# Kernel optimization log

Measured on AMD Instinct MI355X. Metric: run time of the kernel, lower is better.

## Reference

```python
import jax, jax.numpy as jnp
import numpy as np

R_GAS = 8314.46261815324   # Cantera gas constant, J/(kmol K)
ONE_ATM = 101325.0
B, S, NR = 2048, 100, 800
POLY = 5


def setup_inputs() -> dict:
    key = jax.random.key(0)
    ks = jax.random.split(key, 11)
    T = jax.random.uniform(ks[0], (B, 1), minval=300.0, maxval=2500.0)
    P = ONE_ATM * jax.random.uniform(ks[1], (B, 1), minval=0.5, maxval=2.0)
    Y = jax.random.uniform(ks[2], (B, S), minval=0.01, maxval=1.0)
    TPY = jnp.concatenate([T, P, Y], axis=1)
    molecular_weights = jax.random.uniform(ks[3], (S, 1), minval=2.0, maxval=100.0)
    # NASA-7 coefficients with realistic per-column magnitudes
    scales = jnp.array([1.0, 1e-3, 1e-6, 1e-9, 1e-12, 1e3, 1.0])
    base = jnp.array([3.5, 0.0, 0.0, 0.0, 0.0, 0.0, 5.0])
    nasa_low = jax.random.normal(ks[4], (S, 7)) * scales + base
    nasa_high = jax.random.normal(ks[5], (S, 7)) * scales + base
    efficiencies_coeffs = jax.random.uniform(ks[6], (S, NR), minval=0.0, maxval=2.0)
    is_three_body = (jax.random.uniform(ks[7], (NR,)) < 0.3).astype(jnp.float32)
    # positive poly coefficients so viscosity/conductivity/diffusion stay > 0
    species_viscosities_poly = jax.random.uniform(ks[8], (POLY, S), minval=1e-6, maxval=1e-5)
    thermal_conductivity_poly = jax.random.uniform(ks[9], (POLY, S), minval=1e-4, maxval=1e-3)
    binary_diff_coeffs_poly = jax.random.uniform(ks[10], (POLY, S * S), minval=1e-7, maxval=1e-6)
    return {
        'TPY': TPY,
        'molecular_weights': molecular_weights,
        'nasa_low': nasa_low,
        'nasa_high': nasa_high,
        'efficiencies_coeffs': efficiencies_coeffs,
        'is_three_body': is_three_body,
        'species_viscosities_poly': species_viscosities_poly,
        'thermal_conductivity_poly': thermal_conductivity_poly,
        'binary_diff_coeffs_poly': binary_diff_coeffs_poly,
    }


def _forward(TPY, mw, nasa_low, nasa_high, eff, i3b, visc_poly, cond_poly, bdiff_poly):
    n_sp = mw.shape[0]
    # ---- set_states: state variables ----
    T = jnp.clip(TPY[:, 0:1], 200.0, None)            # [B,1]
    logT = jnp.log(T)
    P = TPY[:, 1:2]
    Y = jnp.clip(TPY[:, 2:], 0.0, None)
    Y = Y / Y.sum(axis=1, keepdims=True)
    mean_W = 1.0 / (Y @ (1.0 / mw))                   # [B,1]
    rho = P / R_GAS / T * mean_W                      # mass density
    X = Y * mean_W / mw.T                             # mole fractions
    C = Y * rho / mw.T                                # molar concentrations
    mask = (T <= 1000.0).astype(T.dtype)              # [B,1] NASA branch select
    # ---- cp (NASA poly) ----
    cp_T = jnp.concatenate([T**0, T, T**2, T**3, T**4], axis=1)
    cp = (cp_T @ nasa_low[:, :5].T) * mask + (cp_T @ nasa_high[:, :5].T) * (1.0 - mask)
    cp_mole = (R_GAS * cp * X).sum(axis=1)
    # ---- enthalpy ----
    H_T = jnp.concatenate([T**0, T / 2, T**2 / 3, T**3 / 4, T**4 / 5, 1.0 / T], axis=1)
    H = ((H_T @ nasa_low[:, :6].T) * mask + (H_T @ nasa_high[:, :6].T) * (1.0 - mask)) * R_GAS * T
    h = H / mw.T
    enthalpy_mass = (h * Y).sum(axis=1)
    # ---- entropy ----
    idx = jnp.array([0, 1, 2, 3, 4, 6])
    S_T = jnp.concatenate([logT, T, T**2 / 2, T**3 / 3, T**4 / 4, T**0], axis=1)
    S0 = ((S_T @ nasa_low[:, idx].T) * mask + (S_T @ nasa_high[:, idx].T) * (1.0 - mask)) * R_GAS
    S_sp = S0 - R_GAS * jnp.log(X) - R_GAS * jnp.log(P / ONE_ATM)
    s = S_sp / mw.T
    entropy_mass = (s * Y).sum(axis=1)
    # ---- third-body effective concentrations ----
    C_M = C @ eff                                     # [B,NR]
    C_M2 = C_M * i3b + (1.0 - i3b)
    # ---- update_transport: viscosity (Wilke mixing) ----
    poly_order = visc_poly.shape[0]
    trans_T = jnp.concatenate([logT**i for i in range(poly_order - 1, -1, -1)], axis=1)
    sp_visc = trans_T @ visc_poly                     # [B,S]
    Wk_over_Wj = mw @ (1.0 / mw.T)                    # [S,S]
    Wj_over_Wk = 1.0 / Wk_over_Wj
    eta_ratio = sp_visc[:, :, None] / sp_visc[:, None, :]  # [B,S,S]
    PHI = (1.0 / 2.8284271247461903) / jnp.sqrt(1.0 + Wk_over_Wj) \
          * (1.0 + jnp.sqrt(eta_ratio) * Wj_over_Wk**0.25) ** 2
    denom = jnp.einsum('bij,bj->bi', PHI, X)
    viscosities = (X * sp_visc / denom).sum(axis=1, keepdims=True)
    # ---- thermal conductivity ----
    sp_cond = trans_T @ cond_poly
    thermal_conductivity = 0.5 * ((X * sp_cond).sum(axis=1, keepdims=True)
                                  + 1.0 / (X / sp_cond).sum(axis=1, keepdims=True))
    # ---- mixture-averaged diffusion coefficients ----
    bdc = (trans_T @ bdiff_poly).reshape(-1, n_sp, n_sp)    # [B,S,S]
    X_eps = jnp.clip(X, 1e-12, None)
    XjWj = X_eps @ mw - X_eps * mw.T                        # [B,S]
    XjDjk = jnp.einsum('bj,bjk->bk', X_eps, 1.0 / bdc) \
            - X_eps / jnp.diagonal(bdc, axis1=-2, axis2=-1)
    mix_diff = XjWj / XjDjk / mean_W / P * ONE_ATM
    return jnp.concatenate([cp_mole[:, None], enthalpy_mass[:, None], entropy_mass[:, None],
                            C_M2, viscosities, thermal_conductivity, mix_diff], axis=1)


def reference(TPY, molecular_weights, nasa_low, nasa_high, efficiencies_coeffs,
              is_three_body, species_viscosities_poly, thermal_conductivity_poly,
              binary_diff_coeffs_poly):
    return _forward(TPY, molecular_weights, nasa_low, nasa_high, efficiencies_coeffs,
                    is_three_body, species_viscosities_poly, thermal_conductivity_poly,
                    binary_diff_coeffs_poly)
```

## Files before the change

### kernel.cpp

```cpp
#include <hip/hip_runtime.h>
#include <math.h>

namespace {

constexpr int S = 100;
constexpr int NR = 800;
constexpr int RPB = 4;
constexpr int NTH = 512;
constexpr int IN_COLS = 2 + S;
constexpr int OUT_COLS = 3 + NR + 2 + S;
constexpr float RGASF = 8314.46261815324f;
constexpr float ATMF = 101325.0f;

__device__ __forceinline__ float wave_sum(float v) {
#pragma unroll
  for (int off = 32; off; off >>= 1) v += __shfl_xor(v, off);
  return v;
}

__device__ __forceinline__ float elem(const float4& v, int i) {
  return ((const float*)&v)[i];
}

__global__ __launch_bounds__(NTH, 4)
void chem_props_kernel(const float* __restrict__ TPY,
                       const float* __restrict__ mw,
                       const float* __restrict__ nasa_low,
                       const float* __restrict__ nasa_high,
                       const float* __restrict__ eff,
                       const float* __restrict__ i3b,
                       const float* __restrict__ visc_poly,
                       const float* __restrict__ cond_poly,
                       const float* __restrict__ bdiff_poly,
                       float* __restrict__ out)
{
  __shared__ __align__(16) float4 XL[S];
  __shared__ __align__(16) float4 U1[S];
  __shared__ __align__(16) float4 U2[S];
  __shared__ __align__(16) float4 VL[S];
  __shared__ float mwl[S];
  __shared__ float2 ilm[S];
  __shared__ float pa[8][2];
  __shared__ float pb[8][5];
  __shared__ float rs_L[RPB], rs_cfac[RPB], rs_mW[RPB], rs_scale[RPB], rs_T[RPB];
  __shared__ float psum[2][RPB];

  const int tid = threadIdx.x;
  const int wid = tid >> 6;
  const int lane = tid & 63;
  const int row0 = blockIdx.x * RPB;

  if (tid < S) {
    float m = mw[tid];
    mwl[tid] = m;
    ilm[tid] = make_float2(1.0f / m, __log2f(m));
  }
  __syncthreads();

  const int row = wid & 3;
  const int half = wid >> 2;
  const float* rowp = TPY + (size_t)(row0 + row) * IN_COLS;
  float T = fmaxf(rowp[0], 200.0f);
  float P = rowp[1];
  float L = __logf(T);
  const int s = half * 64 + lane;
  const bool valid = (s < S);
  float y = valid ? fmaxf(rowp[2 + s], 0.0f) : 0.0f;
  float im = valid ? ilm[s].x : 0.0f;
  {
    float py = wave_sum(y);
    float pw = wave_sum(y * im);
    if (lane == 0) { pa[wid][0] = py; pa[wid][1] = pw; }
  }
  __syncthreads();
  {
    float T2 = T * T, T3 = T2 * T, T4 = T2 * T2;
    float invT = 1.0f / T;
    float ysum = pa[row][0] + pa[row + 4][0];
    float wsum = pa[row][1] + pa[row + 4][1];
    float invy = 1.0f / ysum;
    float mW = ysum / wsum;
    float cfac = P / (RGASF * T);
    float lnP = __logf(P * (1.0f / ATMF));
    const float* nasa = (T <= 1000.0f) ? nasa_low : nasa_high;

    float cpx = 0.0f, hy = 0.0f, sy = 0.0f, condA = 0.0f, condB = 0.0f;
    if (valid) {
      float yn = y * invy;
      float x = fmaxf(yn * mW * im, 1e-12f);
      const float* a = nasa + s * 7;
      float a0 = a[0], a1 = a[1], a2 = a[2], a3 = a[3],
            a4 = a[4], a5 = a[5], a6 = a[6];
      float cp = a0 + a1 * T + a2 * T2 + a3 * T3 + a4 * T4;
      float Ht = a0 + 0.5f * a1 * T + (1.0f / 3.0f) * a2 * T2
               + 0.25f * a3 * T3 + 0.2f * a4 * T4 + a5 * invT;
      float S0r = a0 * L + a1 * T + 0.5f * a2 * T2
                + (1.0f / 3.0f) * a3 * T3 + 0.25f * a4 * T4 + a6;
      cpx = cp * x;
      hy = Ht * im * yn;
      sy = (S0r - __logf(x) - lnP) * im * yn;

      float v = visc_poly[0 * S + s];
      v = fmaf(v, L, visc_poly[1 * S + s]);
      v = fmaf(v, L, visc_poly[2 * S + s]);
      v = fmaf(v, L, visc_poly[3 * S + s]);
      v = fmaf(v, L, visc_poly[4 * S + s]);
      float c = cond_poly[0 * S + s];
      c = fmaf(c, L, cond_poly[1 * S + s]);
      c = fmaf(c, L, cond_poly[2 * S + s]);
      c = fmaf(c, L, cond_poly[3 * S + s]);
      c = fmaf(c, L, cond_poly[4 * S + s]);
      condA = x * c;
      condB = x / c;
      ((float*)&XL[s])[row] = x;
      ((float*)&VL[s])[row] = v;
      ((float*)&U1[s])[row] = x * __builtin_amdgcn_rsqf(v);
      ((float*)&U2[s])[row] = x * __builtin_amdgcn_rcpf(v);
    }
    float scp = wave_sum(cpx);
    float sh = wave_sum(hy);
    float ss = wave_sum(sy);
    float sca = wave_sum(condA);
    float scb = wave_sum(condB);
    if (lane == 0) {
      pb[wid][0] = scp; pb[wid][1] = sh; pb[wid][2] = ss;
      pb[wid][3] = sca; pb[wid][4] = scb;
      if (half == 0) {
        rs_L[row] = L;
        rs_T[row] = T;
        rs_cfac[row] = cfac;
        rs_mW[row] = mW;
        rs_scale[row] = ATMF / (mW * P);
      }
    }
  }
  __syncthreads();

  if (tid < RPB) {
    const int r = tid;
    float scp = pb[r][0] + pb[r + 4][0];
    float sh  = pb[r][1] + pb[r + 4][1];
    float ss  = pb[r][2] + pb[r + 4][2];
    float sca = pb[r][3] + pb[r + 4][3];
    float scb = pb[r][4] + pb[r + 4][4];
    float* orow = out + (size_t)(row0 + r) * OUT_COLS;
    orow[0] = RGASF * scp;
    orow[1] = RGASF * rs_T[r] * sh;
    orow[2] = RGASF * ss;
    orow[3 + NR + 1] = 0.5f * (sca + 1.0f / scb);
  }

  if (tid < 200) {
    const int q0 = tid * 4;
    float acc[4][4];
#pragma unroll
    for (int qi = 0; qi < 4; ++qi)
#pragma unroll
      for (int b = 0; b < RPB; ++b) acc[qi][b] = 0.0f;
#pragma unroll 4
    for (int s2 = 0; s2 < S; ++s2) {
      float4 e = *(const float4*)&eff[s2 * NR + q0];
      float4 xq = XL[s2];
#pragma unroll
      for (int qi = 0; qi < 4; ++qi)
#pragma unroll
        for (int b = 0; b < RPB; ++b)
          acc[qi][b] = fmaf(elem(xq, b), elem(e, qi), acc[qi][b]);
    }
    float cf[RPB];
#pragma unroll
    for (int b = 0; b < RPB; ++b) cf[b] = rs_cfac[b];
    float4 t3 = *(const float4*)&i3b[q0];
#pragma unroll
    for (int qi = 0; qi < 4; ++qi) {
      float tq = elem(t3, qi);
      float base = 1.0f - tq;
#pragma unroll
      for (int b = 0; b < RPB; ++b)
        out[(size_t)(row0 + b) * OUT_COLS + 3 + q0 + qi] =
            fmaf(acc[qi][b] * cf[b], tq, base);
    }
  } else if (tid >= 256 && tid < 384) {
    const int i = tid - 256;
    float contrib[RPB] = {0.0f, 0.0f, 0.0f, 0.0f};
    if (i < S) {
      const float mwi = mwl[i];
      const float lmi = ilm[i].y;
      float d0[RPB], d1[RPB], d2[RPB];
#pragma unroll
      for (int b = 0; b < RPB; ++b) { d0[b] = 0; d1[b] = 0; d2[b] = 0; }
#pragma unroll 2
      for (int k = 0; k < S; ++k) {
        float2 il = ilm[k];
        float A = 0.35355339059327373f *
                  __builtin_amdgcn_rsqf(1.0f + mwi * il.x);
        float B4 = __builtin_amdgcn_exp2f(0.25f * (il.y - lmi));
        float m1 = A * B4, m2 = m1 * B4;
        float4 xq = XL[k];
        float4 u1q = U1[k];
        float4 u2q = U2[k];
#pragma unroll
        for (int b = 0; b < RPB; ++b) {
          d0[b] = fmaf(A, elem(xq, b), d0[b]);
          d1[b] = fmaf(m1, elem(u1q, b), d1[b]);
          d2[b] = fmaf(m2, elem(u2q, b), d2[b]);
        }
      }
      float4 vq = VL[i];
      float4 xiq = XL[i];
#pragma unroll
      for (int b = 0; b < RPB; ++b) {
        float vi = elem(vq, b);
        float den = d0[b] + 2.0f * sqrtf(vi) * d1[b] + vi * d2[b];
        contrib[b] = elem(xiq, b) * vi / den;
      }
    }
#pragma unroll
    for (int b = 0; b < RPB; ++b) contrib[b] = wave_sum(contrib[b]);
    if (lane == 0) {
#pragma unroll
      for (int b = 0; b < RPB; ++b) psum[wid - 4][b] = contrib[b];
    }
  } else if (tid >= 384) {
    const int k = tid - 384;
    if (k < S) {
      float Lb[RPB], acc[RPB];
#pragma unroll
      for (int b = 0; b < RPB; ++b) { Lb[b] = rs_L[b]; acc[b] = 0.0f; }
      const float* bp = bdiff_poly + k;
#pragma unroll 2
      for (int j = 0; j < S; ++j) {
        float c0 = bp[j * 100];
        float c1 = bp[10000 + j * 100];
        float c2 = bp[20000 + j * 100];
        float c3 = bp[30000 + j * 100];
        float c4 = bp[40000 + j * 100];
        float4 xq = XL[j];
        bool diag = (j == k);
#pragma unroll
        for (int b = 0; b < RPB; ++b) {
          float p = fmaf(c0, Lb[b], c1);
          p = fmaf(p, Lb[b], c2);
          p = fmaf(p, Lb[b], c3);
          p = fmaf(p, Lb[b], c4);
          float r = diag ? 0.0f : __builtin_amdgcn_rcpf(p);
          acc[b] = fmaf(elem(xq, b), r, acc[b]);
        }
      }
      float4 xkq = XL[k];
      float mwk = mwl[k];
#pragma unroll
      for (int b = 0; b < RPB; ++b) {
        float num = rs_mW[b] - elem(xkq, b) * mwk;
        out[(size_t)(row0 + b) * OUT_COLS + 3 + NR + 2 + k] =
            num * __builtin_amdgcn_rcpf(acc[b]) * rs_scale[b];
      }
    }
  }
  __syncthreads();

  if (tid < RPB) {
    out[(size_t)(row0 + tid) * OUT_COLS + 3 + NR] =
        psum[0][tid] + psum[1][tid];
  }
}

}

extern "C" void kernel_launch(void* const* d_in, const int* in_sizes, int n_in,
                              void* d_out, int out_size, void* d_ws, size_t ws_size,
                              hipStream_t stream) {
  const float* TPY        = (const float*)d_in[0];
  const float* mwp        = (const float*)d_in[1];
  const float* nasa_low   = (const float*)d_in[2];
  const float* nasa_high  = (const float*)d_in[3];
  const float* eff        = (const float*)d_in[4];
  const float* i3b        = (const float*)d_in[5];
  const float* visc_poly  = (const float*)d_in[6];
  const float* cond_poly  = (const float*)d_in[7];
  const float* bdiff_poly = (const float*)d_in[8];
  float* out = (float*)d_out;

  const int B = 2048;
  dim3 grid(B / RPB);
  chem_props_kernel<<<grid, NTH, 0, stream>>>(
      TPY, mwp, nasa_low, nasa_high, eff, i3b,
      visc_poly, cond_poly, bdiff_poly, out);
}
```

Before: 100.0 us.

## Prefetch efficiency and diffusion coefficients into registers with double buffering

Loads the first chunks of the efficiency matrix and the binary-diffusion polynomial coefficients into registers at kernel entry, before the state-setup phase and barriers. The main loops then run over register double buffers, issuing the next chunk's global loads while the current chunk is computed, so global latency overlaps with arithmetic. It also unrolls the viscosity loop further and swaps a division for a hardware reciprocal. The cost is much higher register pressure (about 57 extra floats per thread) under launch_bounds(512,4), which risks spills or lower occupancy.

```diff
diff --git a/kernel.cpp b/kernel.cpp
--- a/kernel.cpp
+++ b/kernel.cpp
@@ -50,6 +50,31 @@
   const int lane = tid & 63;
   const int row0 = blockIdx.x * RPB;
 
+  float4 eA[4], eB[4], t3q;
+  float cA[5][5], cB[5][5];
+  const float* ep = nullptr;
+  const float* bp = nullptr;
+  if (tid < 200) {
+    ep = eff + tid * 4;
+#pragma unroll
+    for (int i = 0; i < 4; ++i) eA[i] = *(const float4*)&ep[(size_t)i * NR];
+#pragma unroll
+    for (int i = 0; i < 4; ++i) eB[i] = *(const float4*)&ep[(size_t)(4 + i) * NR];
+    t3q = *(const float4*)&i3b[tid * 4];
+  } else if (tid >= 384 && tid < 484) {
+    bp = bdiff_poly + (tid - 384);
+#pragma unroll
+    for (int jj = 0; jj < 5; ++jj)
+#pragma unroll
+      for (int d = 0; d < 5; ++d)
+        cA[jj][d] = bp[d * 10000 + jj * 100];
+#pragma unroll
+    for (int jj = 0; jj < 5; ++jj)
+#pragma unroll
+      for (int d = 0; d < 5; ++d)
+        cB[jj][d] = bp[d * 10000 + (5 + jj) * 100];
+  }
+
   if (tid < S) {
     float m = mw[tid];
     mwl[tid] = m;
@@ -157,23 +182,51 @@
     for (int qi = 0; qi < 4; ++qi)
 #pragma unroll
       for (int b = 0; b < RPB; ++b) acc[qi][b] = 0.0f;
-#pragma unroll 4
-    for (int s2 = 0; s2 < S; ++s2) {
-      float4 e = *(const float4*)&eff[s2 * NR + q0];
-      float4 xq = XL[s2];
+
+    for (int g = 0; g < 96; g += 8) {
+#pragma unroll
+      for (int si = 0; si < 4; ++si) {
+        float4 xq = XL[g + si];
+#pragma unroll
+        for (int qi = 0; qi < 4; ++qi)
+#pragma unroll
+          for (int b = 0; b < RPB; ++b)
+            acc[qi][b] = fmaf(elem(xq, b), elem(eA[si], qi), acc[qi][b]);
+      }
+#pragma unroll
+      for (int i = 0; i < 4; ++i)
+        eA[i] = *(const float4*)&ep[(size_t)(g + 8 + i) * NR];
+#pragma unroll
+      for (int si = 0; si < 4; ++si) {
+        float4 xq = XL[g + 4 + si];
+#pragma unroll
+        for (int qi = 0; qi < 4; ++qi)
+#pragma unroll
+          for (int b = 0; b < RPB; ++b)
+            acc[qi][b] = fmaf(elem(xq, b), elem(eB[si], qi), acc[qi][b]);
+      }
+      if (g + 12 < 100) {
+#pragma unroll
+        for (int i = 0; i < 4; ++i)
+          eB[i] = *(const float4*)&ep[(size_t)(g + 12 + i) * NR];
+      }
+    }
+#pragma unroll
+    for (int si = 0; si < 4; ++si) {
+      float4 xq = XL[96 + si];
 #pragma unroll
       for (int qi = 0; qi < 4; ++qi)
 #pragma unroll
         for (int b = 0; b < RPB; ++b)
-          acc[qi][b] = fmaf(elem(xq, b), elem(e, qi), acc[qi][b]);
-    }
+          acc[qi][b] = fmaf(elem(xq, b), elem(eA[si], qi), acc[qi][b]);
+    }
+
     float cf[RPB];
 #pragma unroll
     for (int b = 0; b < RPB; ++b) cf[b] = rs_cfac[b];
-    float4 t3 = *(const float4*)&i3b[q0];
 #pragma unroll
     for (int qi = 0; qi < 4; ++qi) {
-      float tq = elem(t3, qi);
+      float tq = elem(t3q, qi);
       float base = 1.0f - tq;
 #pragma unroll
       for (int b = 0; b < RPB; ++b)
@@ -189,7 +242,7 @@
       float d0[RPB], d1[RPB], d2[RPB];
 #pragma unroll
       for (int b = 0; b < RPB; ++b) { d0[b] = 0; d1[b] = 0; d2[b] = 0; }
-#pragma unroll 2
+#pragma unroll 4
       for (int k = 0; k < S; ++k) {
         float2 il = ilm[k];
         float A = 0.35355339059327373f *
@@ -212,7 +265,7 @@
       for (int b = 0; b < RPB; ++b) {
         float vi = elem(vq, b);
         float den = d0[b] + 2.0f * sqrtf(vi) * d1[b] + vi * d2[b];
-        contrib[b] = elem(xiq, b) * vi / den;
+        contrib[b] = elem(xiq, b) * vi * __builtin_amdgcn_rcpf(den);
       }
     }
 #pragma unroll
@@ -221,40 +274,67 @@
 #pragma unroll
       for (int b = 0; b < RPB; ++b) psum[wid - 4][b] = contrib[b];
     }
-  } else if (tid >= 384) {
+  } else if (tid >= 384 && tid < 484) {
     const int k = tid - 384;
-    if (k < S) {
-      float Lb[RPB], acc[RPB];
-#pragma unroll
-      for (int b = 0; b < RPB; ++b) { Lb[b] = rs_L[b]; acc[b] = 0.0f; }
-      const float* bp = bdiff_poly + k;
-#pragma unroll 2
-      for (int j = 0; j < S; ++j) {
-        float c0 = bp[j * 100];
-        float c1 = bp[10000 + j * 100];
-        float c2 = bp[20000 + j * 100];
-        float c3 = bp[30000 + j * 100];
-        float c4 = bp[40000 + j * 100];
+    float Lb[RPB], acc4[RPB];
+#pragma unroll
+    for (int b = 0; b < RPB; ++b) { Lb[b] = rs_L[b]; acc4[b] = 0.0f; }
+
+    for (int t = 0; t < 20; t += 2) {
+      const int j0 = t * 5;
+#pragma unroll
+      for (int jj = 0; jj < 5; ++jj) {
+        const int j = j0 + jj;
         float4 xq = XL[j];
-        bool diag = (j == k);
+        const bool diag = (j == k);
 #pragma unroll
         for (int b = 0; b < RPB; ++b) {
-          float p = fmaf(c0, Lb[b], c1);
-          p = fmaf(p, Lb[b], c2);
-          p = fmaf(p, Lb[b], c3);
-          p = fmaf(p, Lb[b], c4);
+          float p = fmaf(cA[jj][0], Lb[b], cA[jj][1]);
+          p = fmaf(p, Lb[b], cA[jj][2]);
+          p = fmaf(p, Lb[b], cA[jj][3]);
+          p = fmaf(p, Lb[b], cA[jj][4]);
           float r = diag ? 0.0f : __builtin_amdgcn_rcpf(p);
-          acc[b] = fmaf(elem(xq, b), r, acc[b]);
+          acc4[b] = fmaf(elem(xq, b), r, acc4[b]);
         }
       }
-      float4 xkq = XL[k];
-      float mwk = mwl[k];
-#pragma unroll
-      for (int b = 0; b < RPB; ++b) {
-        float num = rs_mW[b] - elem(xkq, b) * mwk;
-        out[(size_t)(row0 + b) * OUT_COLS + 3 + NR + 2 + k] =
-            num * __builtin_amdgcn_rcpf(acc[b]) * rs_scale[b];
-      }
+      if (t + 2 < 20) {
+#pragma unroll
+        for (int jj = 0; jj < 5; ++jj)
+#pragma unroll
+          for (int d = 0; d < 5; ++d)
+            cA[jj][d] = bp[d * 10000 + ((t + 2) * 5 + jj) * 100];
+      }
+#pragma unroll
+      for (int jj = 0; jj < 5; ++jj) {
+        const int j = j0 + 5 + jj;
+        float4 xq = XL[j];
+        const bool diag = (j == k);
+#pragma unroll
+        for (int b = 0; b < RPB; ++b) {
+          float p = fmaf(cB[jj][0], Lb[b], cB[jj][1]);
+          p = fmaf(p, Lb[b], cB[jj][2]);
+          p = fmaf(p, Lb[b], cB[jj][3]);
+          p = fmaf(p, Lb[b], cB[jj][4]);
+          float r = diag ? 0.0f : __builtin_amdgcn_rcpf(p);
+          acc4[b] = fmaf(elem(xq, b), r, acc4[b]);
+        }
+      }
+      if (t + 3 < 20) {
+#pragma unroll
+        for (int jj = 0; jj < 5; ++jj)
+#pragma unroll
+          for (int d = 0; d < 5; ++d)
+            cB[jj][d] = bp[d * 10000 + ((t + 3) * 5 + jj) * 100];
+      }
+    }
+
+    float4 xkq = XL[k];
+    float mwk = mwl[k];
+#pragma unroll
+    for (int b = 0; b < RPB; ++b) {
+      float num = rs_mW[b] - elem(xkq, b) * mwk;
+      out[(size_t)(row0 + b) * OUT_COLS + 3 + NR + 2 + k] =
+          num * __builtin_amdgcn_rcpf(acc4[b]) * rs_scale[b];
     }
   }
   __syncthreads();
```

After: 149.2 us. 49.2% more time.

## Split each row group across two blocks and precompute viscosity phi table

Applied to the files above, without the earlier changes.

Doubles the grid so that each group of four rows is handled by two blocks. The blocks split the efficiency columns and the diffusion k range between them, and the diffusion j-loop is split across two thread groups that combine partial sums through shared memory. A small pre-kernel fills a species-pair table of the Wilke phi factors in workspace, which removes the rsq, exp2 and log work from the viscosity inner loop. Launch bounds are raised and a divide is replaced with rcp. In exchange, the prologue work is duplicated per block pair, there is an extra launch, and a __syncthreads sits inside a divergent branch followed by an early return.

```diff
diff --git a/kernel.cpp b/kernel.cpp
--- a/kernel.cpp
+++ b/kernel.cpp
@@ -11,6 +11,7 @@
 constexpr int OUT_COLS = 3 + NR + 2 + S;
 constexpr float RGASF = 8314.46261815324f;
 constexpr float ATMF = 101325.0f;
+constexpr size_t PHI_WS_BYTES = 3 * 10000 * sizeof(float);
 
 __device__ __forceinline__ float wave_sum(float v) {
 #pragma unroll
@@ -22,7 +23,22 @@
   return ((const float*)&v)[i];
 }
 
-__global__ __launch_bounds__(NTH, 4)
+__global__ __launch_bounds__(256)
+void phi_precompute(const float* __restrict__ mw, float* __restrict__ pm) {
+  int idx = blockIdx.x * 256 + threadIdx.x;
+  if (idx >= 10000) return;
+  int i = idx / 100, k = idx % 100;
+  float mwi = mw[i], mwk = mw[k];
+  float A = 0.35355339059327373f *
+            __builtin_amdgcn_rsqf(1.0f + mwi * __builtin_amdgcn_rcpf(mwk));
+  float B4 = __builtin_amdgcn_exp2f(0.25f * (__log2f(mwk) - __log2f(mwi)));
+  pm[idx] = A;
+  pm[10000 + idx] = A * B4;
+  pm[20000 + idx] = A * B4 * B4;
+}
+
+template <bool PRE>
+__global__ __launch_bounds__(NTH, 8)
 void chem_props_kernel(const float* __restrict__ TPY,
                        const float* __restrict__ mw,
                        const float* __restrict__ nasa_low,
@@ -32,6 +48,7 @@
                        const float* __restrict__ visc_poly,
                        const float* __restrict__ cond_poly,
                        const float* __restrict__ bdiff_poly,
+                       const float* __restrict__ pm,
                        float* __restrict__ out)
 {
   __shared__ __align__(16) float4 XL[S];
@@ -44,11 +61,13 @@
   __shared__ float pb[8][5];
   __shared__ float rs_L[RPB], rs_cfac[RPB], rs_mW[RPB], rs_scale[RPB], rs_T[RPB];
   __shared__ float psum[2][RPB];
+  __shared__ __align__(16) float xjd[50][RPB];
 
   const int tid = threadIdx.x;
   const int wid = tid >> 6;
   const int lane = tid & 63;
-  const int row0 = blockIdx.x * RPB;
+  const int h = blockIdx.x & 1;
+  const int row0 = (blockIdx.x >> 1) * RPB;
 
   if (tid < S) {
     float m = mw[tid];
@@ -136,7 +155,7 @@
   }
   __syncthreads();
 
-  if (tid < RPB) {
+  if (h == 0 && tid < RPB) {
     const int r = tid;
     float scp = pb[r][0] + pb[r + 4][0];
     float sh  = pb[r][1] + pb[r + 4][1];
@@ -151,59 +170,81 @@
   }
 
   if (tid < 200) {
-    const int q0 = tid * 4;
-    float acc[4][4];
-#pragma unroll
-    for (int qi = 0; qi < 4; ++qi)
+    const int q0 = h * 400 + tid * 2;
+    float acc[2][RPB];
+#pragma unroll
+    for (int qi = 0; qi < 2; ++qi)
 #pragma unroll
       for (int b = 0; b < RPB; ++b) acc[qi][b] = 0.0f;
 #pragma unroll 4
     for (int s2 = 0; s2 < S; ++s2) {
-      float4 e = *(const float4*)&eff[s2 * NR + q0];
+      float2 e = *(const float2*)&eff[(size_t)s2 * NR + q0];
       float4 xq = XL[s2];
 #pragma unroll
-      for (int qi = 0; qi < 4; ++qi)
-#pragma unroll
-        for (int b = 0; b < RPB; ++b)
-          acc[qi][b] = fmaf(elem(xq, b), elem(e, qi), acc[qi][b]);
-    }
-    float cf[RPB];
-#pragma unroll
-    for (int b = 0; b < RPB; ++b) cf[b] = rs_cfac[b];
-    float4 t3 = *(const float4*)&i3b[q0];
-#pragma unroll
-    for (int qi = 0; qi < 4; ++qi) {
-      float tq = elem(t3, qi);
+      for (int b = 0; b < RPB; ++b) {
+        acc[0][b] = fmaf(elem(xq, b), e.x, acc[0][b]);
+        acc[1][b] = fmaf(elem(xq, b), e.y, acc[1][b]);
+      }
+    }
+    float2 t3 = *(const float2*)&i3b[q0];
+#pragma unroll
+    for (int qi = 0; qi < 2; ++qi) {
+      float tq = qi ? t3.y : t3.x;
       float base = 1.0f - tq;
 #pragma unroll
       for (int b = 0; b < RPB; ++b)
         out[(size_t)(row0 + b) * OUT_COLS + 3 + q0 + qi] =
-            fmaf(acc[qi][b] * cf[b], tq, base);
-    }
-  } else if (tid >= 256 && tid < 384) {
+            fmaf(acc[qi][b] * rs_cfac[b], tq, base);
+    }
+  } else if (tid >= 256 && tid < 384 && h == 0) {
     const int i = tid - 256;
     float contrib[RPB] = {0.0f, 0.0f, 0.0f, 0.0f};
     if (i < S) {
-      const float mwi = mwl[i];
-      const float lmi = ilm[i].y;
       float d0[RPB], d1[RPB], d2[RPB];
 #pragma unroll
       for (int b = 0; b < RPB; ++b) { d0[b] = 0; d1[b] = 0; d2[b] = 0; }
+      if (PRE) {
+        const float* pm0 = pm + i * 100;
+        const float* pm1 = pm + 10000 + i * 100;
+        const float* pm2 = pm + 20000 + i * 100;
 #pragma unroll 2
-      for (int k = 0; k < S; ++k) {
-        float2 il = ilm[k];
-        float A = 0.35355339059327373f *
-                  __builtin_amdgcn_rsqf(1.0f + mwi * il.x);
-        float B4 = __builtin_amdgcn_exp2f(0.25f * (il.y - lmi));
-        float m1 = A * B4, m2 = m1 * B4;
-        float4 xq = XL[k];
-        float4 u1q = U1[k];
-        float4 u2q = U2[k];
-#pragma unroll
-        for (int b = 0; b < RPB; ++b) {
-          d0[b] = fmaf(A, elem(xq, b), d0[b]);
-          d1[b] = fmaf(m1, elem(u1q, b), d1[b]);
-          d2[b] = fmaf(m2, elem(u2q, b), d2[b]);
+        for (int k4 = 0; k4 < S; k4 += 4) {
+          float4 a0q = *(const float4*)&pm0[k4];
+          float4 a1q = *(const float4*)&pm1[k4];
+          float4 a2q = *(const float4*)&pm2[k4];
+#pragma unroll
+          for (int kk = 0; kk < 4; ++kk) {
+            float4 xq = XL[k4 + kk];
+            float4 u1q = U1[k4 + kk];
+            float4 u2q = U2[k4 + kk];
+            float m0 = elem(a0q, kk), m1 = elem(a1q, kk), m2 = elem(a2q, kk);
+#pragma unroll
+            for (int b = 0; b < RPB; ++b) {
+              d0[b] = fmaf(m0, elem(xq, b), d0[b]);
+              d1[b] = fmaf(m1, elem(u1q, b), d1[b]);
+              d2[b] = fmaf(m2, elem(u2q, b), d2[b]);
+            }
+          }
+        }
+      } else {
+        const float mwi = mwl[i];
+        const float lmi = ilm[i].y;
+#pragma unroll 4
+        for (int k = 0; k < S; ++k) {
+          float2 il = ilm[k];
+          float A = 0.35355339059327373f *
+                    __builtin_amdgcn_rsqf(1.0f + mwi * il.x);
+          float B4 = __builtin_amdgcn_exp2f(0.25f * (il.y - lmi));
+          float m1 = A * B4, m2 = m1 * B4;
+          float4 xq = XL[k];
+          float4 u1q = U1[k];
+          float4 u2q = U2[k];
+#pragma unroll
+          for (int b = 0; b < RPB; ++b) {
+            d0[b] = fmaf(A, elem(xq, b), d0[b]);
+            d1[b] = fmaf(m1, elem(u1q, b), d1[b]);
+            d2[b] = fmaf(m2, elem(u2q, b), d2[b]);
+          }
         }
       }
       float4 vq = VL[i];
@@ -212,7 +253,7 @@
       for (int b = 0; b < RPB; ++b) {
         float vi = elem(vq, b);
         float den = d0[b] + 2.0f * sqrtf(vi) * d1[b] + vi * d2[b];
-        contrib[b] = elem(xiq, b) * vi / den;
+        contrib[b] = elem(xiq, b) * vi * __builtin_amdgcn_rcpf(den);
       }
     }
 #pragma unroll
@@ -221,45 +262,59 @@
 #pragma unroll
       for (int b = 0; b < RPB; ++b) psum[wid - 4][b] = contrib[b];
     }
-  } else if (tid >= 384) {
-    const int k = tid - 384;
-    if (k < S) {
-      float Lb[RPB], acc[RPB];
-#pragma unroll
-      for (int b = 0; b < RPB; ++b) { Lb[b] = rs_L[b]; acc[b] = 0.0f; }
-      const float* bp = bdiff_poly + k;
+  } else if (tid >= 384 && tid < 484) {
+    const int td = tid - 384;
+    const int kk = td % 50;
+    const int jh = td / 50;
+    const int k = h * 50 + kk;
+    const int j0 = jh * 50;
+    float Lb[RPB], acc4[RPB];
+#pragma unroll
+    for (int b = 0; b < RPB; ++b) { Lb[b] = rs_L[b]; acc4[b] = 0.0f; }
+    const float* bp = bdiff_poly + k;
 #pragma unroll 2
-      for (int j = 0; j < S; ++j) {
-        float c0 = bp[j * 100];
-        float c1 = bp[10000 + j * 100];
-        float c2 = bp[20000 + j * 100];
-        float c3 = bp[30000 + j * 100];
-        float c4 = bp[40000 + j * 100];
-        float4 xq = XL[j];
-        bool diag = (j == k);
-#pragma unroll
-        for (int b = 0; b < RPB; ++b) {
-          float p = fmaf(c0, Lb[b], c1);
-          p = fmaf(p, Lb[b], c2);
-          p = fmaf(p, Lb[b], c3);
-          p = fmaf(p, Lb[b], c4);
-          float r = diag ? 0.0f : __builtin_amdgcn_rcpf(p);
-          acc[b] = fmaf(elem(xq, b), r, acc[b]);
-        }
-      }
+    for (int j = j0; j < j0 + 50; ++j) {
+      float c0 = bp[j * 100];
+      float c1 = bp[10000 + j * 100];
+      float c2 = bp[20000 + j * 100];
+      float c3 = bp[30000 + j * 100];
+      float c4 = bp[40000 + j * 100];
+      float4 xq = XL[j];
+      const bool diag = (j == k);
+#pragma unroll
+      for (int b = 0; b < RPB; ++b) {
+        float p = fmaf(c0, Lb[b], c1);
+        p = fmaf(p, Lb[b], c2);
+        p = fmaf(p, Lb[b], c3);
+        p = fmaf(p, Lb[b], c4);
+        float r = diag ? 0.0f : __builtin_amdgcn_rcpf(p);
+        acc4[b] = fmaf(elem(xq, b), r, acc4[b]);
+      }
+    }
+    if (jh == 0) {
+#pragma unroll
+      for (int b = 0; b < RPB; ++b) xjd[kk][b] = acc4[b];
+    } else {
+#pragma unroll
+      for (int b = 0; b < RPB; ++b) Lb[b] = acc4[b];
+    }
+    __syncthreads();
+    if (jh == 1) {
       float4 xkq = XL[k];
       float mwk = mwl[k];
 #pragma unroll
       for (int b = 0; b < RPB; ++b) {
+        float tot = xjd[kk][b] + Lb[b];
         float num = rs_mW[b] - elem(xkq, b) * mwk;
         out[(size_t)(row0 + b) * OUT_COLS + 3 + NR + 2 + k] =
-            num * __builtin_amdgcn_rcpf(acc[b]) * rs_scale[b];
-      }
-    }
+            num * __builtin_amdgcn_rcpf(tot) * rs_scale[b];
+      }
+    }
+    return;
   }
   __syncthreads();
 
-  if (tid < RPB) {
+  if (h == 0 && tid < RPB) {
     out[(size_t)(row0 + tid) * OUT_COLS + 3 + NR] =
         psum[0][tid] + psum[1][tid];
   }
@@ -280,10 +335,18 @@
   const float* cond_poly  = (const float*)d_in[7];
   const float* bdiff_poly = (const float*)d_in[8];
   float* out = (float*)d_out;
+  float* pm  = (float*)d_ws;
 
   const int B = 2048;
-  dim3 grid(B / RPB);
-  chem_props_kernel<<<grid, NTH, 0, stream>>>(
-      TPY, mwp, nasa_low, nasa_high, eff, i3b,
-      visc_poly, cond_poly, bdiff_poly, out);
-}
+  dim3 grid((B / RPB) * 2);
+  if (ws_size >= PHI_WS_BYTES) {
+    phi_precompute<<<40, 256, 0, stream>>>(mwp, pm);
+    chem_props_kernel<true><<<grid, NTH, 0, stream>>>(
+        TPY, mwp, nasa_low, nasa_high, eff, i3b,
+        visc_poly, cond_poly, bdiff_poly, pm, out);
+  } else {
+    chem_props_kernel<false><<<grid, NTH, 0, stream>>>(
+        TPY, mwp, nasa_low, nasa_high, eff, i3b,
+        visc_poly, cond_poly, bdiff_poly, nullptr, out);
+  }
+}
```

New measurement: 121.2 us. +21.2%, slower.
